# Performance work log

Hardware: AMD Instinct MI355X
Metric: run time of the kernel (lower is better)

The kernel has to match this reference:

```python
import jax, jax.numpy as jnp
import numpy as np
from math import sqrt

B, L, D_MODEL = 4, 128, 256
V, D_WORD = 50257, 768
H = 8  # n_heads; d_keys = D_MODEL // H = 32


def setup_inputs() -> dict:
    key = jax.random.key(0)
    ks = jax.random.split(key, 10)
    s = lambda k, shape, fan: jax.random.normal(k, shape, dtype=jnp.float32) / np.sqrt(fan)
    return {
        "time_series_embedding": jax.random.normal(ks[0], (B, L, D_MODEL), dtype=jnp.float32),
        "word_embedding": jax.random.normal(ks[1], (V, D_WORD), dtype=jnp.float32) * 0.02,
        "Wq": s(ks[2], (D_MODEL, D_MODEL), D_MODEL),
        "bq": jnp.zeros((D_MODEL,), jnp.float32),
        "Wk": s(ks[3], (D_WORD, D_MODEL), D_WORD),
        "bk": jnp.zeros((D_MODEL,), jnp.float32),
        "Wv": s(ks[4], (D_WORD, D_MODEL), D_WORD),
        "bv": jnp.zeros((D_MODEL,), jnp.float32),
        "Wo": s(ks[5], (D_MODEL, D_MODEL), D_MODEL),
        "bo": jnp.zeros((D_MODEL,), jnp.float32),
    }


def reference(time_series_embedding, word_embedding, Wq, bq, Wk, bk, Wv, bv, Wo, bo):
    b, l, _ = time_series_embedding.shape
    v, _ = word_embedding.shape
    h = H
    e = D_MODEL // h
    # projections
    query = (time_series_embedding @ Wq + bq).reshape(b, l, h, e)   # [B,L,H,E]
    key = (word_embedding @ Wk + bk).reshape(v, h, e)               # [V,H,E]
    value = (word_embedding @ Wv + bv).reshape(v, h, e)             # [V,H,E]
    scale = 1.0 / sqrt(e)
    # scores over full vocab: [B,H,V,L]
    scores = jnp.einsum('blhe,vhe->bhvl', query, key)
    # NOTE: faithful to source -- softmax over the LAST axis (l, the query dim)
    attn = jax.nn.softmax(scale * scores, axis=-1)
    # dropout is identity in eval mode
    reprog = jnp.einsum('bhvl,vhe->blhe', attn, value).reshape(b, l, h * e)
    return reprog @ Wo + bo  # [B,L,d_model]
```

## Files before the change

kernel.cpp:

```cpp
#include <hip/hip_runtime.h>
#include <hip/hip_bf16.h>
#include <string.h>

#define BB 4
#define LL 128
#define DM 256
#define VV 50257
#define VPAD 50304
#define DW 768
#define HH 8
#define EE 32

typedef __attribute__((ext_vector_type(8))) short sh8;
typedef __attribute__((ext_vector_type(4))) float f32x4;

static __device__ inline unsigned short bfbits(float x) {
  __hip_bfloat16 h = __float2bfloat16(x);
  unsigned short u;
  __builtin_memcpy(&u, &h, 2);
  return u;
}

__global__ __launch_bounds__(256) void qproj_kernel(
    const float* __restrict__ tse, const float* __restrict__ Wq,
    const float* __restrict__ bq, unsigned short* __restrict__ Qb) {
  __shared__ float row[DM];
  int r = blockIdx.x;
  int n = threadIdx.x;
  row[n] = tse[r * DM + n];
  __syncthreads();
  float acc = bq[n];
#pragma unroll 8
  for (int k = 0; k < DM; ++k)
    acc = fmaf(row[k], Wq[k * DM + n], acc);
  const float scale = 0.17677669529663687f;
  Qb[r * DM + n] = bfbits(acc * scale);
}

__global__ __launch_bounds__(256) void wtrans_kernel(
    const float* __restrict__ Wk, const float* __restrict__ Wv,
    unsigned short* __restrict__ Wkt, unsigned short* __restrict__ Wvt) {
  int bx = blockIdx.x;
  const float* src = (bx & 1) ? Wv : Wk;
  unsigned short* dst = (bx & 1) ? Wvt : Wkt;
  int n = bx >> 1;
  int t = threadIdx.x;
#pragma unroll
  for (int j = 0; j < 3; ++j) {
    int k = t + 256 * j;
    dst[(size_t)n * DW + k] = bfbits(src[(size_t)k * DM + n]);
  }
}

#define KST 40
__global__ __launch_bounds__(256, 2) void kvproj_kernel(
    const float* __restrict__ WE, const unsigned short* __restrict__ Wkt,
    const unsigned short* __restrict__ Wvt, const float* __restrict__ bk,
    const float* __restrict__ bv, unsigned short* __restrict__ Kb,
    unsigned short* __restrict__ Vb) {
  __shared__ short WEb[128 * KST];
  __shared__ short Wkb[128 * KST];
  __shared__ short Wvb[128 * KST];

  int bx = blockIdx.x;
  int v0 = (bx >> 1) * 128;
  int colbase = (bx & 1) * 128;
  int t = threadIdx.x;
  int w = t >> 6, lane = t & 63, a = lane & 15, quad = lane >> 4;
  int wm = w >> 1, wn = w & 1;

  int sr = t >> 1;
  int skc = (t & 1) * 16;

  f32x4 Ck[4][4], Cv[4][4];
#pragma unroll
  for (int mb = 0; mb < 4; ++mb)
#pragma unroll
    for (int nb = 0; nb < 4; ++nb) {
      Ck[mb][nb] = (f32x4){0.f, 0.f, 0.f, 0.f};
      Cv[mb][nb] = (f32x4){0.f, 0.f, 0.f, 0.f};
    }

  for (int kt = 0; kt < 24; ++kt) {
    int vrow = v0 + sr;
    float4 a0, a1, a2, a3;
    if (vrow < VV) {
      const float* wep = WE + (size_t)vrow * DW + kt * 32 + skc;
      a0 = *(const float4*)(wep + 0);
      a1 = *(const float4*)(wep + 4);
      a2 = *(const float4*)(wep + 8);
      a3 = *(const float4*)(wep + 12);
    } else {
      a0 = a1 = a2 = a3 = (float4){0.f, 0.f, 0.f, 0.f};
    }
    const unsigned short* kp = Wkt + (size_t)(colbase + sr) * DW + kt * 32 + skc;
    const unsigned short* vp = Wvt + (size_t)(colbase + sr) * DW + kt * 32 + skc;
    sh8 k0 = *(const sh8*)(kp + 0);
    sh8 k1 = *(const sh8*)(kp + 8);
    sh8 x0 = *(const sh8*)(vp + 0);
    sh8 x1 = *(const sh8*)(vp + 8);

    __syncthreads();

    sh8 p0, p1;
    p0[0] = (short)bfbits(a0.x); p0[1] = (short)bfbits(a0.y);
    p0[2] = (short)bfbits(a0.z); p0[3] = (short)bfbits(a0.w);
    p0[4] = (short)bfbits(a1.x); p0[5] = (short)bfbits(a1.y);
    p0[6] = (short)bfbits(a1.z); p0[7] = (short)bfbits(a1.w);
    p1[0] = (short)bfbits(a2.x); p1[1] = (short)bfbits(a2.y);
    p1[2] = (short)bfbits(a2.z); p1[3] = (short)bfbits(a2.w);
    p1[4] = (short)bfbits(a3.x); p1[5] = (short)bfbits(a3.y);
    p1[6] = (short)bfbits(a3.z); p1[7] = (short)bfbits(a3.w);
    *(sh8*)&WEb[sr * KST + skc] = p0;
    *(sh8*)&WEb[sr * KST + skc + 8] = p1;
    *(sh8*)&Wkb[sr * KST + skc] = k0;
    *(sh8*)&Wkb[sr * KST + skc + 8] = k1;
    *(sh8*)&Wvb[sr * KST + skc] = x0;
    *(sh8*)&Wvb[sr * KST + skc + 8] = x1;
    __syncthreads();

    sh8 A[4], Bk[4], Bv[4];
#pragma unroll
    for (int mb = 0; mb < 4; ++mb)
      A[mb] = *(const sh8*)&WEb[(wm * 64 + mb * 16 + a) * KST + quad * 8];
#pragma unroll
    for (int nb = 0; nb < 4; ++nb) {
      Bk[nb] = *(const sh8*)&Wkb[((wn * 4 + nb) * 16 + a) * KST + quad * 8];
      Bv[nb] = *(const sh8*)&Wvb[((wn * 4 + nb) * 16 + a) * KST + quad * 8];
    }
#pragma unroll
    for (int mb = 0; mb < 4; ++mb)
#pragma unroll
      for (int nb = 0; nb < 4; ++nb) {
        Ck[mb][nb] = __builtin_amdgcn_mfma_f32_16x16x32_bf16(
            A[mb], Bk[nb], Ck[mb][nb], 0, 0, 0);
        Cv[mb][nb] = __builtin_amdgcn_mfma_f32_16x16x32_bf16(
            A[mb], Bv[nb], Cv[mb][nb], 0, 0, 0);
      }
  }

  float bkv[4], bvv[4];
#pragma unroll
  for (int nb = 0; nb < 4; ++nb) {
    int n = colbase + (wn * 4 + nb) * 16 + a;
    bkv[nb] = bk[n];
    bvv[nb] = bv[n];
  }
#pragma unroll
  for (int mb = 0; mb < 4; ++mb)
#pragma unroll
    for (int nb = 0; nb < 4; ++nb)
#pragma unroll
      for (int r = 0; r < 4; ++r) {
        int m = v0 + wm * 64 + mb * 16 + quad * 4 + r;
        int n = colbase + (wn * 4 + nb) * 16 + a;
        bool live = m < VV;
        Kb[(size_t)m * DM + n] = live ? bfbits(Ck[mb][nb][r] + bkv[nb]) : 0;
        Vb[(size_t)m * DM + n] = live ? bfbits(Cv[mb][nb][r] + bvv[nb]) : 0;
      }
}

__global__ void zero_kernel(float* __restrict__ p, int n) {
  int i = blockIdx.x * blockDim.x + threadIdx.x;
  if (i < n) p[i] = 0.f;
}

#define PST 72
__global__ __launch_bounds__(256) void attn_kernel(
    const unsigned short* __restrict__ Qb, const unsigned short* __restrict__ Kb,
    const unsigned short* __restrict__ Vb, float* __restrict__ reprog, int bpb) {
  __shared__ short Pb[LL * PST];
  __shared__ short Vt[EE * PST];

  int bh = blockIdx.x / bpb;
  int chunk = blockIdx.x - bh * bpb;
  int b = bh >> 3, h = bh & 7;
  int t = threadIdx.x;
  int w = t >> 6;
  int lane = t & 63;
  int a = lane & 15;
  int quad = lane >> 4;

  sh8 qf[8];
  const unsigned short* qbase = Qb + (size_t)(b * LL) * DM + h * EE;
#pragma unroll
  for (int tau = 0; tau < 8; ++tau)
    qf[tau] = *(const sh8*)(qbase + (size_t)(tau * 16 + a) * DM + quad * 8);

  f32x4 C[2][2];
#pragma unroll
  for (int mb = 0; mb < 2; ++mb)
#pragma unroll
    for (int nb = 0; nb < 2; ++nb)
      C[mb][nb] = (f32x4){0.f, 0.f, 0.f, 0.f};

  const int ntiles = VPAD >> 6;
  for (int tile = chunk; tile < ntiles; tile += bpb) {
    int v0 = tile << 6;
    __syncthreads();

    sh8 af = *(const sh8*)(Kb + (size_t)(v0 + 16 * w + a) * DM + h * EE + quad * 8);
    int vr = t >> 2, e0 = (t & 3) * 8;
    sh8 vv = *(const sh8*)(Vb + (size_t)(v0 + vr) * DM + h * EE + e0);

    f32x4 S[8];
#pragma unroll
    for (int tau = 0; tau < 8; ++tau) {
      f32x4 z = {0.f, 0.f, 0.f, 0.f};
      S[tau] = __builtin_amdgcn_mfma_f32_16x16x32_bf16(af, qf[tau], z, 0, 0, 0);
    }

    float mx[4], sm[4], inv[4];
#pragma unroll
    for (int r = 0; r < 4; ++r) {
      float m = S[0][r];
#pragma unroll
      for (int tau = 1; tau < 8; ++tau) m = fmaxf(m, S[tau][r]);
      mx[r] = m;
    }
#pragma unroll
    for (int msk = 1; msk <= 8; msk <<= 1)
#pragma unroll
      for (int r = 0; r < 4; ++r)
        mx[r] = fmaxf(mx[r], __shfl_xor(mx[r], msk));
#pragma unroll
    for (int r = 0; r < 4; ++r) sm[r] = 0.f;
#pragma unroll
    for (int tau = 0; tau < 8; ++tau)
#pragma unroll
      for (int r = 0; r < 4; ++r) {
        float ex = __expf(S[tau][r] - mx[r]);
        S[tau][r] = ex;
        sm[r] += ex;
      }
#pragma unroll
    for (int msk = 1; msk <= 8; msk <<= 1)
#pragma unroll
      for (int r = 0; r < 4; ++r)
        sm[r] += __shfl_xor(sm[r], msk);
#pragma unroll
    for (int r = 0; r < 4; ++r) inv[r] = 1.f / sm[r];

    {
      const short* vs = (const short*)&vv;
#pragma unroll
      for (int j = 0; j < 8; ++j)
        Vt[(e0 + j) * PST + vr] = vs[j];
    }
#pragma unroll
    for (int tau = 0; tau < 8; ++tau) {
      ushort4 pk;
      pk.x = bfbits(S[tau][0] * inv[0]);
      pk.y = bfbits(S[tau][1] * inv[1]);
      pk.z = bfbits(S[tau][2] * inv[2]);
      pk.w = bfbits(S[tau][3] * inv[3]);
      *(ushort4*)&Pb[(tau * 16 + a) * PST + 16 * w + quad * 4] = pk;
    }
    __syncthreads();

    sh8 Afr[2][2], Bfr[2][2];
#pragma unroll
    for (int mb = 0; mb < 2; ++mb)
#pragma unroll
      for (int kb = 0; kb < 2; ++kb)
        Afr[mb][kb] =
            *(const sh8*)&Pb[(32 * w + mb * 16 + a) * PST + kb * 32 + quad * 8];
#pragma unroll
    for (int kb = 0; kb < 2; ++kb)
#pragma unroll
      for (int nb = 0; nb < 2; ++nb)
        Bfr[kb][nb] = *(const sh8*)&Vt[(nb * 16 + a) * PST + kb * 32 + quad * 8];
#pragma unroll
    for (int kb = 0; kb < 2; ++kb)
#pragma unroll
      for (int mb = 0; mb < 2; ++mb)
#pragma unroll
        for (int nb = 0; nb < 2; ++nb)
          C[mb][nb] = __builtin_amdgcn_mfma_f32_16x16x32_bf16(
              Afr[mb][kb], Bfr[kb][nb], C[mb][nb], 0, 0, 0);
  }

#pragma unroll
  for (int mb = 0; mb < 2; ++mb)
#pragma unroll
    for (int nb = 0; nb < 2; ++nb)
#pragma unroll
      for (int r = 0; r < 4; ++r) {
        int l = 32 * w + mb * 16 + quad * 4 + r;
        int e = nb * 16 + a;
        atomicAdd(&reprog[(size_t)(b * LL + l) * DM + h * EE + e], C[mb][nb][r]);
      }
}

__global__ __launch_bounds__(256) void outproj_kernel(
    const float* __restrict__ reprog, const float* __restrict__ Wo,
    const float* __restrict__ bo, float* __restrict__ out) {
  __shared__ float row[DM];
  int r = blockIdx.x, n = threadIdx.x;
  row[n] = reprog[r * DM + n];
  __syncthreads();
  float acc = bo[n];
#pragma unroll 8
  for (int k = 0; k < DM; ++k)
    acc = fmaf(row[k], Wo[k * DM + n], acc);
  out[r * DM + n] = acc;
}

extern "C" void kernel_launch(void* const* d_in, const int* in_sizes, int n_in,
                              void* d_out, int out_size, void* d_ws, size_t ws_size,
                              hipStream_t stream) {
  const float* tse = (const float*)d_in[0];
  const float* WE  = (const float*)d_in[1];
  const float* Wq  = (const float*)d_in[2];
  const float* bq  = (const float*)d_in[3];
  const float* Wk  = (const float*)d_in[4];
  const float* bk  = (const float*)d_in[5];
  const float* Wv  = (const float*)d_in[6];
  const float* bv  = (const float*)d_in[7];
  const float* Wo  = (const float*)d_in[8];
  const float* bo  = (const float*)d_in[9];
  float* out = (float*)d_out;

  char* ws = (char*)d_ws;
  const size_t QB_BYTES = (size_t)BB * LL * DM * 2;
  const size_t KV_BYTES = (size_t)VPAD * DM * 2;
  const size_t WT_BYTES = (size_t)DM * DW * 2;
  unsigned short* Qb  = (unsigned short*)ws;
  unsigned short* Kb  = (unsigned short*)(ws + QB_BYTES);
  unsigned short* Vb  = (unsigned short*)(ws + QB_BYTES + KV_BYTES);
  char* X = ws + QB_BYTES + 2 * KV_BYTES;
  unsigned short* Wkt = (unsigned short*)X;
  unsigned short* Wvt = (unsigned short*)(X + WT_BYTES);
  float* reprog = (float*)X;

  const int BPB = 32;

  wtrans_kernel<<<2 * DM, 256, 0, stream>>>(Wk, Wv, Wkt, Wvt);
  qproj_kernel<<<BB * LL, 256, 0, stream>>>(tse, Wq, bq, Qb);
  kvproj_kernel<<<(VPAD / 128) * 2, 256, 0, stream>>>(WE, Wkt, Wvt, bk, bv, Kb, Vb);
  zero_kernel<<<(BB * LL * DM + 255) / 256, 256, 0, stream>>>(reprog, BB * LL * DM);
  attn_kernel<<<32 * BPB, 256, 0, stream>>>(Qb, Kb, Vb, reprog, BPB);
  outproj_kernel<<<BB * LL, 256, 0, stream>>>(reprog, Wo, bo, out);
}
```

Measured before the change: 440.3 us.

## Prefetch next tiles in KV-projection and attention loops, tile weight transpose via LDS

The KV projection kernel now issues the global loads for the next K-step right after the LDS stores, so they are in flight during the current MFMA work. The LDS row stride changes from 40 to 36 shorts, with LDS accesses split into 64-bit pieces to cut bank conflicts. The attention kernel likewise prefetches the next tile's K and V fragments during the PV MFMA phase, with the barrier moved accordingly. The weight transpose kernel uses a padded 64x64 shared-memory tile so both reads and writes are coalesced. This costs more live registers, which may hurt occupancy.

```diff
diff --git a/kernel.cpp b/kernel.cpp
--- a/kernel.cpp
+++ b/kernel.cpp
@@ -12,6 +12,7 @@
 #define EE 32
 
 typedef __attribute__((ext_vector_type(8))) short sh8;
+typedef __attribute__((ext_vector_type(4))) short sh4;
 typedef __attribute__((ext_vector_type(4))) float f32x4;
 
 static __device__ inline unsigned short bfbits(float x) {
@@ -19,6 +20,12 @@
   unsigned short u;
   __builtin_memcpy(&u, &h, 2);
   return u;
+}
+
+static __device__ inline sh8 ld8_b64(const short* p) {
+  sh4 lo = *(const sh4*)p;
+  sh4 hi = *(const sh4*)(p + 4);
+  return __builtin_shufflevector(lo, hi, 0, 1, 2, 3, 4, 5, 6, 7);
 }
 
 __global__ __launch_bounds__(256) void qproj_kernel(
@@ -40,27 +47,34 @@
 __global__ __launch_bounds__(256) void wtrans_kernel(
     const float* __restrict__ Wk, const float* __restrict__ Wv,
     unsigned short* __restrict__ Wkt, unsigned short* __restrict__ Wvt) {
-  int bx = blockIdx.x;
-  const float* src = (bx & 1) ? Wv : Wk;
-  unsigned short* dst = (bx & 1) ? Wvt : Wkt;
-  int n = bx >> 1;
+  __shared__ float tileS[64][65];
+  const float* src = blockIdx.z ? Wv : Wk;
+  unsigned short* dst = blockIdx.z ? Wvt : Wkt;
+  int k0 = blockIdx.x * 64, n0 = blockIdx.y * 64;
   int t = threadIdx.x;
-#pragma unroll
-  for (int j = 0; j < 3; ++j) {
-    int k = t + 256 * j;
-    dst[(size_t)n * DW + k] = bfbits(src[(size_t)k * DM + n]);
-  }
-}
-
-#define KST 40
+  int c = t & 63, rb = t >> 6;
+#pragma unroll
+  for (int j = 0; j < 16; ++j) {
+    int r = j * 4 + rb;
+    tileS[r][c] = src[(size_t)(k0 + r) * DM + n0 + c];
+  }
+  __syncthreads();
+#pragma unroll
+  for (int j = 0; j < 16; ++j) {
+    int r = j * 4 + rb;
+    dst[(size_t)(n0 + r) * DW + k0 + c] = bfbits(tileS[c][r]);
+  }
+}
+
+#define KST2 36
 __global__ __launch_bounds__(256, 2) void kvproj_kernel(
     const float* __restrict__ WE, const unsigned short* __restrict__ Wkt,
     const unsigned short* __restrict__ Wvt, const float* __restrict__ bk,
     const float* __restrict__ bv, unsigned short* __restrict__ Kb,
     unsigned short* __restrict__ Vb) {
-  __shared__ short WEb[128 * KST];
-  __shared__ short Wkb[128 * KST];
-  __shared__ short Wvb[128 * KST];
+  __shared__ short WEb[128 * KST2];
+  __shared__ short Wkb[128 * KST2];
+  __shared__ short Wvb[128 * KST2];
 
   int bx = blockIdx.x;
   int v0 = (bx >> 1) * 128;
@@ -68,24 +82,16 @@
   int t = threadIdx.x;
   int w = t >> 6, lane = t & 63, a = lane & 15, quad = lane >> 4;
   int wm = w >> 1, wn = w & 1;
-
   int sr = t >> 1;
   int skc = (t & 1) * 16;
-
-  f32x4 Ck[4][4], Cv[4][4];
-#pragma unroll
-  for (int mb = 0; mb < 4; ++mb)
-#pragma unroll
-    for (int nb = 0; nb < 4; ++nb) {
-      Ck[mb][nb] = (f32x4){0.f, 0.f, 0.f, 0.f};
-      Cv[mb][nb] = (f32x4){0.f, 0.f, 0.f, 0.f};
-    }
-
-  for (int kt = 0; kt < 24; ++kt) {
-    int vrow = v0 + sr;
-    float4 a0, a1, a2, a3;
-    if (vrow < VV) {
-      const float* wep = WE + (size_t)vrow * DW + kt * 32 + skc;
+  const bool live = (v0 + sr) < VV;
+
+  float4 a0, a1, a2, a3;
+  sh8 k0, k1, x0, x1;
+
+  auto issue_loads = [&](int kt) {
+    if (live) {
+      const float* wep = WE + (size_t)(v0 + sr) * DW + kt * 32 + skc;
       a0 = *(const float4*)(wep + 0);
       a1 = *(const float4*)(wep + 4);
       a2 = *(const float4*)(wep + 8);
@@ -95,38 +101,63 @@
     }
     const unsigned short* kp = Wkt + (size_t)(colbase + sr) * DW + kt * 32 + skc;
     const unsigned short* vp = Wvt + (size_t)(colbase + sr) * DW + kt * 32 + skc;
-    sh8 k0 = *(const sh8*)(kp + 0);
-    sh8 k1 = *(const sh8*)(kp + 8);
-    sh8 x0 = *(const sh8*)(vp + 0);
-    sh8 x1 = *(const sh8*)(vp + 8);
-
+    k0 = *(const sh8*)(kp + 0);
+    k1 = *(const sh8*)(kp + 8);
+    x0 = *(const sh8*)(vp + 0);
+    x1 = *(const sh8*)(vp + 8);
+  };
+
+  f32x4 Ck[4][4], Cv[4][4];
+#pragma unroll
+  for (int mb = 0; mb < 4; ++mb)
+#pragma unroll
+    for (int nb = 0; nb < 4; ++nb) {
+      Ck[mb][nb] = (f32x4){0.f, 0.f, 0.f, 0.f};
+      Cv[mb][nb] = (f32x4){0.f, 0.f, 0.f, 0.f};
+    }
+
+  issue_loads(0);
+
+  for (int kt = 0; kt < 24; ++kt) {
     __syncthreads();
 
-    sh8 p0, p1;
-    p0[0] = (short)bfbits(a0.x); p0[1] = (short)bfbits(a0.y);
-    p0[2] = (short)bfbits(a0.z); p0[3] = (short)bfbits(a0.w);
-    p0[4] = (short)bfbits(a1.x); p0[5] = (short)bfbits(a1.y);
-    p0[6] = (short)bfbits(a1.z); p0[7] = (short)bfbits(a1.w);
-    p1[0] = (short)bfbits(a2.x); p1[1] = (short)bfbits(a2.y);
-    p1[2] = (short)bfbits(a2.z); p1[3] = (short)bfbits(a2.w);
-    p1[4] = (short)bfbits(a3.x); p1[5] = (short)bfbits(a3.y);
-    p1[6] = (short)bfbits(a3.z); p1[7] = (short)bfbits(a3.w);
-    *(sh8*)&WEb[sr * KST + skc] = p0;
-    *(sh8*)&WEb[sr * KST + skc + 8] = p1;
-    *(sh8*)&Wkb[sr * KST + skc] = k0;
-    *(sh8*)&Wkb[sr * KST + skc + 8] = k1;
-    *(sh8*)&Wvb[sr * KST + skc] = x0;
-    *(sh8*)&Wvb[sr * KST + skc + 8] = x1;
+    {
+      sh4 w0 = {(short)bfbits(a0.x), (short)bfbits(a0.y),
+                (short)bfbits(a0.z), (short)bfbits(a0.w)};
+      sh4 w1 = {(short)bfbits(a1.x), (short)bfbits(a1.y),
+                (short)bfbits(a1.z), (short)bfbits(a1.w)};
+      sh4 w2 = {(short)bfbits(a2.x), (short)bfbits(a2.y),
+                (short)bfbits(a2.z), (short)bfbits(a2.w)};
+      sh4 w3 = {(short)bfbits(a3.x), (short)bfbits(a3.y),
+                (short)bfbits(a3.z), (short)bfbits(a3.w)};
+      short* eb = &WEb[sr * KST2 + skc];
+      *(sh4*)(eb + 0) = w0;
+      *(sh4*)(eb + 4) = w1;
+      *(sh4*)(eb + 8) = w2;
+      *(sh4*)(eb + 12) = w3;
+      short* kb = &Wkb[sr * KST2 + skc];
+      *(sh4*)(kb + 0) = __builtin_shufflevector(k0, k0, 0, 1, 2, 3);
+      *(sh4*)(kb + 4) = __builtin_shufflevector(k0, k0, 4, 5, 6, 7);
+      *(sh4*)(kb + 8) = __builtin_shufflevector(k1, k1, 0, 1, 2, 3);
+      *(sh4*)(kb + 12) = __builtin_shufflevector(k1, k1, 4, 5, 6, 7);
+      short* vb = &Wvb[sr * KST2 + skc];
+      *(sh4*)(vb + 0) = __builtin_shufflevector(x0, x0, 0, 1, 2, 3);
+      *(sh4*)(vb + 4) = __builtin_shufflevector(x0, x0, 4, 5, 6, 7);
+      *(sh4*)(vb + 8) = __builtin_shufflevector(x1, x1, 0, 1, 2, 3);
+      *(sh4*)(vb + 12) = __builtin_shufflevector(x1, x1, 4, 5, 6, 7);
+    }
     __syncthreads();
 
+    if (kt < 23) issue_loads(kt + 1);
+
     sh8 A[4], Bk[4], Bv[4];
 #pragma unroll
     for (int mb = 0; mb < 4; ++mb)
-      A[mb] = *(const sh8*)&WEb[(wm * 64 + mb * 16 + a) * KST + quad * 8];
+      A[mb] = ld8_b64(&WEb[(wm * 64 + mb * 16 + a) * KST2 + quad * 8]);
 #pragma unroll
     for (int nb = 0; nb < 4; ++nb) {
-      Bk[nb] = *(const sh8*)&Wkb[((wn * 4 + nb) * 16 + a) * KST + quad * 8];
-      Bv[nb] = *(const sh8*)&Wvb[((wn * 4 + nb) * 16 + a) * KST + quad * 8];
+      Bk[nb] = ld8_b64(&Wkb[((wn * 4 + nb) * 16 + a) * KST2 + quad * 8]);
+      Bv[nb] = ld8_b64(&Wvb[((wn * 4 + nb) * 16 + a) * KST2 + quad * 8]);
     }
 #pragma unroll
     for (int mb = 0; mb < 4; ++mb)
@@ -154,9 +185,9 @@
       for (int r = 0; r < 4; ++r) {
         int m = v0 + wm * 64 + mb * 16 + quad * 4 + r;
         int n = colbase + (wn * 4 + nb) * 16 + a;
-        bool live = m < VV;
-        Kb[(size_t)m * DM + n] = live ? bfbits(Ck[mb][nb][r] + bkv[nb]) : 0;
-        Vb[(size_t)m * DM + n] = live ? bfbits(Cv[mb][nb][r] + bvv[nb]) : 0;
+        bool ok = m < VV;
+        Kb[(size_t)m * DM + n] = ok ? bfbits(Ck[mb][nb][r] + bkv[nb]) : 0;
+        Vb[(size_t)m * DM + n] = ok ? bfbits(Cv[mb][nb][r] + bvv[nb]) : 0;
       }
 }
 
@@ -180,6 +211,7 @@
   int lane = t & 63;
   int a = lane & 15;
   int quad = lane >> 4;
+  int vr = t >> 2, e0 = (t & 3) * 8;
 
   sh8 qf[8];
   const unsigned short* qbase = Qb + (size_t)(b * LL) * DM + h * EE;
@@ -195,14 +227,15 @@
       C[mb][nb] = (f32x4){0.f, 0.f, 0.f, 0.f};
 
   const int ntiles = VPAD >> 6;
+
+  sh8 af, vv;
+  {
+    int v0 = chunk << 6;
+    af = *(const sh8*)(Kb + (size_t)(v0 + 16 * w + a) * DM + h * EE + quad * 8);
+    vv = *(const sh8*)(Vb + (size_t)(v0 + vr) * DM + h * EE + e0);
+  }
+
   for (int tile = chunk; tile < ntiles; tile += bpb) {
-    int v0 = tile << 6;
-    __syncthreads();
-
-    sh8 af = *(const sh8*)(Kb + (size_t)(v0 + 16 * w + a) * DM + h * EE + quad * 8);
-    int vr = t >> 2, e0 = (t & 3) * 8;
-    sh8 vv = *(const sh8*)(Vb + (size_t)(v0 + vr) * DM + h * EE + e0);
-
     f32x4 S[8];
 #pragma unroll
     for (int tau = 0; tau < 8; ++tau) {
@@ -240,6 +273,8 @@
         sm[r] += __shfl_xor(sm[r], msk);
 #pragma unroll
     for (int r = 0; r < 4; ++r) inv[r] = 1.f / sm[r];
+
+    __syncthreads();
 
     {
       const short* vs = (const short*)&vv;
@@ -257,6 +292,13 @@
       *(ushort4*)&Pb[(tau * 16 + a) * PST + 16 * w + quad * 4] = pk;
     }
     __syncthreads();
+
+    int nt = tile + bpb;
+    if (nt < ntiles) {
+      int v0n = nt << 6;
+      af = *(const sh8*)(Kb + (size_t)(v0n + 16 * w + a) * DM + h * EE + quad * 8);
+      vv = *(const sh8*)(Vb + (size_t)(v0n + vr) * DM + h * EE + e0);
+    }
 
     sh8 Afr[2][2], Bfr[2][2];
 #pragma unroll
@@ -335,7 +377,7 @@
 
   const int BPB = 32;
 
-  wtrans_kernel<<<2 * DM, 256, 0, stream>>>(Wk, Wv, Wkt, Wvt);
+  wtrans_kernel<<<dim3(DW / 64, DM / 64, 2), 256, 0, stream>>>(Wk, Wv, Wkt, Wvt);
   qproj_kernel<<<BB * LL, 256, 0, stream>>>(tse, Wq, bq, Qb);
   kvproj_kernel<<<(VPAD / 128) * 2, 256, 0, stream>>>(WE, Wkt, Wvt, bk, bv, Kb, Vb);
   zero_kernel<<<(BB * LL * DM + 255) / 256, 256, 0, stream>>>(reprog, BB * LL * DM);
```

New measurement: 419.7 us. -4.7%, faster.
